# Performance work log

Measured on AMD Instinct MI355X. Metric: run time of the kernel, lower is better.

The kernel has to match this reference:

```python
import jax, jax.numpy as jnp
import numpy as np

F_FEAT = 310   # len(feature_names)
B = 2048       # samples; x has F_FEAT*B elements
H = 32         # sfp_neurons


def _uniform(key, shape, bound):
    return jax.random.uniform(key, shape, jnp.float32, -bound, bound)


def setup_inputs() -> dict:
    key = jax.random.key(0)
    ks = jax.random.split(key, 7)
    x = jax.random.normal(ks[0], (F_FEAT, B), dtype=jnp.float32)
    # Stacked per-feature MLP params (torch Linear default init: U(-1/sqrt(fan_in), +)).
    s1 = 1.0 / np.sqrt(F_FEAT - 1)
    s2 = 1.0 / np.sqrt(H)
    W1 = _uniform(ks[1], (F_FEAT, F_FEAT - 1, H), s1)  # (in, out) layout
    b1 = _uniform(ks[2], (F_FEAT, H), s1)
    W2 = _uniform(ks[3], (F_FEAT, H, H), s2)
    b2 = _uniform(ks[4], (F_FEAT, H), s2)
    W3 = _uniform(ks[5], (F_FEAT, H, H), s2)
    b3 = _uniform(ks[6], (F_FEAT, H), s2)
    return {"x": x, "W1": W1, "b1": b1, "W2": W2, "b2": b2, "W3": W3, "b3": b3}


def reference(x, W1, b1, W2, b2, W3, b3):
    F_, B_ = x.shape
    # Leave-one-out gather: for SFP i, rows [0..i-1, i+1..F-1] of x (feature-major),
    # then the original's view(-1, 1, F-1) reinterprets the flat buffer as (B, F-1).
    idx = jnp.arange(F_ - 1)[None, :]
    idx = idx + (idx >= jnp.arange(F_)[:, None])          # (F, F-1)
    X = x[idx].reshape(F_, B_, F_ - 1)                    # (F, B, F-1) grouped inputs
    h = jax.nn.relu(jnp.einsum('fbk,fkh->fbh', X, W1) + b1[:, None, :])
    h = jax.nn.relu(jnp.einsum('fbh,fhg->fbg', h, W2) + b2[:, None, :])
    h = jax.nn.relu(jnp.einsum('fbh,fhg->fbg', h, W3) + b3[:, None, :])  # (F, B, H)
    # torch.cat of per-SFP .view(-1) == row-major flatten of (F, B, H)
    return h.reshape(-1)
```

## Files before the change

kernel.cpp:

```cpp
#include <hip/hip_runtime.h>

namespace {

constexpr int F_FEAT = 310;
constexpr int KDIM   = 309;
constexpr int BSZ    = 2048;
constexpr int HDIM   = 32;
constexpr int NCH    = 10;
constexpr int NX     = F_FEAT * BSZ;

constexpr int    NBLK8    = NX / 8 + 2;
constexpr size_t CSTR_B   = (size_t)NBLK8 * 16;
constexpr size_t XC_BYTES = CSTR_B * 8;
constexpr size_t W1T_FSTR = 32 * 320 * 2;
constexpr size_t W1T_OFF  = XC_BYTES;
constexpr size_t W2T_OFF  = W1T_OFF + (size_t)F_FEAT * W1T_FSTR;
constexpr size_t WT_FSTR  = 32 * 32 * 2;
constexpr size_t W3T_OFF  = W2T_OFF + (size_t)F_FEAT * WT_FSTR;
constexpr size_t WS_NEED  = W3T_OFF + (size_t)F_FEAT * WT_FSTR;

constexpr int NBX      = (NBLK8 + 255) / 256;
constexpr int CVT_XBLK = NBX * 8;
constexpr int CVT_BLK  = CVT_XBLK + F_FEAT * 6;

typedef __bf16 bf16x8 __attribute__((ext_vector_type(8)));
typedef float  f32x4  __attribute__((ext_vector_type(4)));

#define MFMA(a, b, c) __builtin_amdgcn_mfma_f32_16x16x32_bf16((a), (b), (c), 0, 0, 0)

__global__ __launch_bounds__(256) void cvt_all(
    const float* __restrict__ x,  const float* __restrict__ W1,
    const float* __restrict__ W2, const float* __restrict__ W3,
    char* __restrict__ ws)
{
    __shared__ float tile[64][33];
    const int b = blockIdx.x, tid = threadIdx.x;

    if (b < CVT_XBLK) {
        const int c = b / NBX, mb = b - c * NBX;
        const int m = mb * 256 + tid;
        if (m >= NBLK8) return;
        const int e0 = m * 8 - c;
        bf16x8 v;
        #pragma unroll
        for (int q = 0; q < 8; ++q) {
            const int i = e0 + q;
            v[q] = (__bf16)((i >= 0 && i < NX) ? x[i] : 0.f);
        }
        *(bf16x8*)(ws + (size_t)c * CSTR_B + (size_t)m * 16) = v;
        return;
    }

    const int wb = b - CVT_XBLK;
    const int fi = wb / 6, part = wb - fi * 6;

    if (part < 5) {
        const float* Wg = W1 + (size_t)fi * KDIM * HDIM;
        const int row = tid >> 2;
        const int c8  = (tid & 3) * 8;
        const int k   = part * 64 + row;
        float4 f0 = make_float4(0,0,0,0), f1 = f0;
        if (k < KDIM) {
            f0 = *(const float4*)&Wg[k * HDIM + c8];
            f1 = *(const float4*)&Wg[k * HDIM + c8 + 4];
        }
        tile[row][c8+0] = f0.x; tile[row][c8+1] = f0.y;
        tile[row][c8+2] = f0.z; tile[row][c8+3] = f0.w;
        tile[row][c8+4] = f1.x; tile[row][c8+5] = f1.y;
        tile[row][c8+6] = f1.z; tile[row][c8+7] = f1.w;
        __syncthreads();
        const int h = tid & 31, kq = (tid >> 5) * 8;
        bf16x8 o;
        #pragma unroll
        for (int j = 0; j < 8; ++j) o[j] = (__bf16)tile[kq + j][h];
        const int boff = (h * 640 + part * 128 + kq * 2) ^ ((h & 7) << 4);
        *(bf16x8*)(ws + W1T_OFF + (size_t)fi * W1T_FSTR + (size_t)boff) = o;
    } else {
        const int kl = tid >> 3, h4 = (tid & 7) * 4;
        const int h = tid & 31, kq = (tid >> 5) * 8;
        {
            const float* Wg = W2 + (size_t)fi * HDIM * HDIM;
            float4 f = *(const float4*)&Wg[kl * HDIM + h4];
            tile[kl][h4+0] = f.x; tile[kl][h4+1] = f.y;
            tile[kl][h4+2] = f.z; tile[kl][h4+3] = f.w;
            __syncthreads();
            if (tid < 128) {
                bf16x8 o;
                #pragma unroll
                for (int j = 0; j < 8; ++j) o[j] = (__bf16)tile[kq + j][h];
                *(bf16x8*)(ws + W2T_OFF + (size_t)fi * WT_FSTR + (size_t)(h * 32 + kq) * 2) = o;
            }
            __syncthreads();
        }
        {
            const float* Wg = W3 + (size_t)fi * HDIM * HDIM;
            float4 f = *(const float4*)&Wg[kl * HDIM + h4];
            tile[kl][h4+0] = f.x; tile[kl][h4+1] = f.y;
            tile[kl][h4+2] = f.z; tile[kl][h4+3] = f.w;
            __syncthreads();
            if (tid < 128) {
                bf16x8 o;
                #pragma unroll
                for (int j = 0; j < 8; ++j) o[j] = (__bf16)tile[kq + j][h];
                *(bf16x8*)(ws + W3T_OFF + (size_t)fi * WT_FSTR + (size_t)(h * 32 + kq) * 2) = o;
            }
        }
    }
}

template<bool FAST>
__global__ __launch_bounds__(256, 4) void sfp3(
    const float* __restrict__ x,
    const float* __restrict__ W1, const float* __restrict__ b1,
    const float* __restrict__ W2, const float* __restrict__ b2,
    const float* __restrict__ W3, const float* __restrict__ b3,
    const char* __restrict__ ws, float* __restrict__ out)
{
    __shared__ __attribute__((aligned(16))) __bf16 W1s[32 * 320];
    __shared__ __attribute__((aligned(16))) __bf16 h1s[128 * 40];

    int fi, sb;
    if (FAST) {
        const int xc = blockIdx.x & 7, li = blockIdx.x >> 3;
        const int cnt = (xc < 6) ? 39 : 38;
        const int lf = li >> 4;
        if (lf >= cnt) return;
        fi = ((xc < 6) ? xc * 39 : 234 + (xc - 6) * 38) + lf;
        sb = li & 15;
    } else {
        fi = blockIdx.x >> 4; sb = blockIdx.x & 15;
    }

    const int tid = threadIdx.x, lane = tid & 63, wv = tid >> 6;
    const int l15 = lane & 15, l16 = lane >> 4;
    const int lk8 = l16 * 8, r0 = l16 * 4;
    const int b0 = sb << 7, iB = fi << 11;

    if (FAST) {
        const char* src = ws + W1T_OFF + (size_t)fi * W1T_FSTR;
        #pragma unroll
        for (int i = 0; i < 5; ++i) {
            const int off = i * 4096 + tid * 16;
            *(bf16x8*)((char*)W1s + off) = *(const bf16x8*)(src + off);
        }
        __syncthreads();
    }

    const float b1v0 = b1[fi*HDIM + l15], b1v1 = b1[fi*HDIM + 16 + l15];
    const float b2v0 = b2[fi*HDIM + l15], b2v1 = b2[fi*HDIM + 16 + l15];
    const float b3v0 = b3[fi*HDIM + l15], b3v1 = b3[fi*HDIM + 16 + l15];

    bf16x8 w2a, w2b, w3a, w3b;
    if (FAST) {
        const char* p2 = ws + W2T_OFF + (size_t)fi * WT_FSTR;
        const char* p3 = ws + W3T_OFF + (size_t)fi * WT_FSTR;
        w2a = *(const bf16x8*)(p2 + (size_t)(l15 * 32 + lk8) * 2);
        w2b = *(const bf16x8*)(p2 + (size_t)((16 + l15) * 32 + lk8) * 2);
        w3a = *(const bf16x8*)(p3 + (size_t)(l15 * 32 + lk8) * 2);
        w3b = *(const bf16x8*)(p3 + (size_t)((16 + l15) * 32 + lk8) * 2);
    } else {
        #pragma unroll
        for (int q = 0; q < 8; ++q) {
            const size_t base = (size_t)fi * HDIM * HDIM + (lk8 + q) * HDIM;
            w2a[q] = (__bf16)W2[base + l15];      w2b[q] = (__bf16)W2[base + 16 + l15];
            w3a[q] = (__bf16)W3[base + l15];      w3b[q] = (__bf16)W3[base + 16 + l15];
        }
    }

    const int mrow = wv * 32;
    const int lin0 = (b0 + mrow + l15) * KDIM + lk8;
    const int lin1 = lin0 + 16 * KDIM;
    const char* base0 = ws;
    const char* base1 = ws;
    if (FAST) {
        const int c80 = (-lin0) & 7, c81 = (-lin1) & 7;
        base0 = ws + (size_t)c80 * CSTR_B + (size_t)(lin0 + c80) * 2;
        base1 = ws + (size_t)c81 * CSTR_B + (size_t)(lin1 + c81) * 2;
    }

    auto fragA = [&](const char* base, int lin) -> bf16x8 {
        if (FAST) {
            if (__builtin_expect((unsigned)(iB - 1 - lin) < 7u, 0)) {
                bf16x8 r;
                #pragma unroll
                for (int q = 0; q < 8; ++q) {
                    int i = lin + q; i += (i >= iB) ? BSZ : 0;
                    r[q] = *(const __bf16*)(ws + (size_t)i * 2);
                }
                return r;
            }
            return *(const bf16x8*)(base + ((lin >= iB) ? 4096 : 0));
        } else {
            bf16x8 r;
            #pragma unroll
            for (int q = 0; q < 8; ++q) {
                int i = lin + q; i += (i >= iB) ? BSZ : 0;
                i = (i < NX) ? i : (NX - 1);
                r[q] = (__bf16)x[i];
            }
            return r;
        }
    };

    auto fragW1 = [&](int c, int hrow) -> bf16x8 {
        if (FAST) {
            const int boff = (hrow * 640 + c * 64 + l16 * 16) ^ ((hrow & 7) << 4);
            return *(const bf16x8*)((const char*)W1s + boff);
        } else {
            const float* Wg = W1 + (size_t)fi * KDIM * HDIM;
            bf16x8 r;
            #pragma unroll
            for (int q = 0; q < 8; ++q) {
                const int k = c * 32 + lk8 + q;
                r[q] = (__bf16)((k < KDIM) ? Wg[k * HDIM + hrow] : 0.f);
            }
            return r;
        }
    };

    f32x4 acc00 = {0,0,0,0}, acc01 = {0,0,0,0}, acc10 = {0,0,0,0}, acc11 = {0,0,0,0};

    bf16x8 aC0 = fragA(base0,      lin0);
    bf16x8 aC1 = fragA(base1,      lin1);
    bf16x8 aN0 = fragA(base0 + 64, lin0 + 32);
    bf16x8 aN1 = fragA(base1 + 64, lin1 + 32);
    #pragma unroll
    for (int c = 0; c < NCH; ++c) {
        bf16x8 aF0, aF1;
        if (c + 2 < NCH) {
            aF0 = fragA(base0 + 64 * (c + 2), lin0 + 32 * (c + 2));
            aF1 = fragA(base1 + 64 * (c + 2), lin1 + 32 * (c + 2));
        }
        bf16x8 w0 = fragW1(c, l15), w1 = fragW1(c, 16 + l15);
        acc00 = MFMA(aC0, w0, acc00);
        acc01 = MFMA(aC0, w1, acc01);
        acc10 = MFMA(aC1, w0, acc10);
        acc11 = MFMA(aC1, w1, acc11);
        aC0 = aN0; aC1 = aN1; aN0 = aF0; aN1 = aF1;
    }

    constexpr int LDA = 40;
    #pragma unroll
    for (int r = 0; r < 4; ++r) {
        float v;
        v = acc00[r] + b1v0; h1s[(mrow +      r0 + r)*LDA +      l15] = (__bf16)(v > 0.f ? v : 0.f);
        v = acc01[r] + b1v1; h1s[(mrow +      r0 + r)*LDA + 16 + l15] = (__bf16)(v > 0.f ? v : 0.f);
        v = acc10[r] + b1v0; h1s[(mrow + 16 + r0 + r)*LDA +      l15] = (__bf16)(v > 0.f ? v : 0.f);
        v = acc11[r] + b1v1; h1s[(mrow + 16 + r0 + r)*LDA + 16 + l15] = (__bf16)(v > 0.f ? v : 0.f);
    }

    const f32x4 z = {0,0,0,0};
    f32x4 c200, c201, c210, c211;
    {
        bf16x8 ha0 = *(const bf16x8*)&h1s[(mrow +      l15)*LDA + lk8];
        bf16x8 ha1 = *(const bf16x8*)&h1s[(mrow + 16 + l15)*LDA + lk8];
        c200 = MFMA(ha0, w2a, z); c201 = MFMA(ha0, w2b, z);
        c210 = MFMA(ha1, w2a, z); c211 = MFMA(ha1, w2b, z);
    }
    #pragma unroll
    for (int r = 0; r < 4; ++r) {
        float v;
        v = c200[r] + b2v0; h1s[(mrow +      r0 + r)*LDA +      l15] = (__bf16)(v > 0.f ? v : 0.f);
        v = c201[r] + b2v1; h1s[(mrow +      r0 + r)*LDA + 16 + l15] = (__bf16)(v > 0.f ? v : 0.f);
        v = c210[r] + b2v0; h1s[(mrow + 16 + r0 + r)*LDA +      l15] = (__bf16)(v > 0.f ? v : 0.f);
        v = c211[r] + b2v1; h1s[(mrow + 16 + r0 + r)*LDA + 16 + l15] = (__bf16)(v > 0.f ? v : 0.f);
    }

    f32x4 c300, c301, c310, c311;
    {
        bf16x8 ha0 = *(const bf16x8*)&h1s[(mrow +      l15)*LDA + lk8];
        bf16x8 ha1 = *(const bf16x8*)&h1s[(mrow + 16 + l15)*LDA + lk8];
        c300 = MFMA(ha0, w3a, z); c301 = MFMA(ha0, w3b, z);
        c310 = MFMA(ha1, w3a, z); c311 = MFMA(ha1, w3b, z);
    }

    const size_t orow = (size_t)(fi * BSZ + b0 + mrow);
    #pragma unroll
    for (int r = 0; r < 4; ++r) {
        float v;
        v = c300[r] + b3v0; out[(orow +      r0 + r)*HDIM +      l15] = v > 0.f ? v : 0.f;
        v = c301[r] + b3v1; out[(orow +      r0 + r)*HDIM + 16 + l15] = v > 0.f ? v : 0.f;
        v = c310[r] + b3v0; out[(orow + 16 + r0 + r)*HDIM +      l15] = v > 0.f ? v : 0.f;
        v = c311[r] + b3v1; out[(orow + 16 + r0 + r)*HDIM + 16 + l15] = v > 0.f ? v : 0.f;
    }
}

}

extern "C" void kernel_launch(void* const* d_in, const int* in_sizes, int n_in,
                              void* d_out, int out_size, void* d_ws, size_t ws_size,
                              hipStream_t stream) {
    const float* x  = (const float*)d_in[0];
    const float* W1 = (const float*)d_in[1];
    const float* b1 = (const float*)d_in[2];
    const float* W2 = (const float*)d_in[3];
    const float* b2 = (const float*)d_in[4];
    const float* W3 = (const float*)d_in[5];
    const float* b3 = (const float*)d_in[6];
    float* out = (float*)d_out;
    char* ws = (char*)d_ws;

    const bool fast = (ws != nullptr) && (ws_size >= WS_NEED);
    if (fast) {
        hipLaunchKernelGGL(cvt_all, dim3(CVT_BLK), dim3(256), 0, stream, x, W1, W2, W3, ws);
        hipLaunchKernelGGL((sfp3<true>), dim3(8 * 39 * 16), dim3(256), 0, stream,
                           x, W1, b1, W2, b2, W3, b3, ws, out);
    } else {
        hipLaunchKernelGGL((sfp3<false>), dim3(F_FEAT * 16), dim3(256), 0, stream,
                           x, W1, b1, W2, b2, W3, b3, ws, out);
    }
}
```

Measured before the change: 70.93 us.

## Double rows per block to amortize W1 staging and weight loads

Each block now covers 256 samples instead of 128, so each wave computes four 16-row M tiles instead of two. The per-feature W1 copy into shared memory and the W2/W3 fragment loads are amortized over twice the work, and the grid is halved. The A-fragment prefetch depth drops from two chunks to one. In exchange, register pressure rises from 8 accumulators plus more A fragments, shared memory for h1 doubles, and the smaller grid gives fewer blocks to hide latency.

```diff
diff --git a/kernel.cpp b/kernel.cpp
--- a/kernel.cpp
+++ b/kernel.cpp
@@ -109,7 +109,7 @@
 }
 
 template<bool FAST>
-__global__ __launch_bounds__(256, 4) void sfp3(
+__global__ __launch_bounds__(256, 4) void sfp4(
     const float* __restrict__ x,
     const float* __restrict__ W1, const float* __restrict__ b1,
     const float* __restrict__ W2, const float* __restrict__ b2,
@@ -117,24 +117,25 @@
     const char* __restrict__ ws, float* __restrict__ out)
 {
     __shared__ __attribute__((aligned(16))) __bf16 W1s[32 * 320];
-    __shared__ __attribute__((aligned(16))) __bf16 h1s[128 * 40];
+    __shared__ __attribute__((aligned(16))) __bf16 h1s[256 * 40];
 
     int fi, sb;
     if (FAST) {
         const int xc = blockIdx.x & 7, li = blockIdx.x >> 3;
         const int cnt = (xc < 6) ? 39 : 38;
-        const int lf = li >> 4;
+        const int lf = li >> 3;
         if (lf >= cnt) return;
         fi = ((xc < 6) ? xc * 39 : 234 + (xc - 6) * 38) + lf;
-        sb = li & 15;
+        sb = li & 7;
     } else {
-        fi = blockIdx.x >> 4; sb = blockIdx.x & 15;
+        fi = blockIdx.x >> 3; sb = blockIdx.x & 7;
     }
 
     const int tid = threadIdx.x, lane = tid & 63, wv = tid >> 6;
     const int l15 = lane & 15, l16 = lane >> 4;
     const int lk8 = l16 * 8, r0 = l16 * 4;
-    const int b0 = sb << 7, iB = fi << 11;
+    const int b0 = sb << 8, iB = fi << 11;
+    const int mrow = wv * 64;
 
     if (FAST) {
         const char* src = ws + W1T_OFF + (size_t)fi * W1T_FSTR;
@@ -167,34 +168,36 @@
         }
     }
 
-    const int mrow = wv * 32;
-    const int lin0 = (b0 + mrow + l15) * KDIM + lk8;
-    const int lin1 = lin0 + 16 * KDIM;
-    const char* base0 = ws;
-    const char* base1 = ws;
-    if (FAST) {
-        const int c80 = (-lin0) & 7, c81 = (-lin1) & 7;
-        base0 = ws + (size_t)c80 * CSTR_B + (size_t)(lin0 + c80) * 2;
-        base1 = ws + (size_t)c81 * CSTR_B + (size_t)(lin1 + c81) * 2;
-    }
-
-    auto fragA = [&](const char* base, int lin) -> bf16x8 {
+    int lin[4];
+    const char* base[4];
+    #pragma unroll
+    for (int m = 0; m < 4; ++m) {
+        lin[m] = (b0 + mrow + 16 * m + l15) * KDIM + lk8;
         if (FAST) {
-            if (__builtin_expect((unsigned)(iB - 1 - lin) < 7u, 0)) {
+            const int c8 = (-lin[m]) & 7;
+            base[m] = ws + (size_t)c8 * CSTR_B + (size_t)(lin[m] + c8) * 2;
+        } else {
+            base[m] = ws;
+        }
+    }
+
+    auto fragA = [&](const char* bp, int li_) -> bf16x8 {
+        if (FAST) {
+            if (__builtin_expect((unsigned)(iB - 1 - li_) < 7u, 0)) {
                 bf16x8 r;
                 #pragma unroll
                 for (int q = 0; q < 8; ++q) {
-                    int i = lin + q; i += (i >= iB) ? BSZ : 0;
+                    int i = li_ + q; i += (i >= iB) ? BSZ : 0;
                     r[q] = *(const __bf16*)(ws + (size_t)i * 2);
                 }
                 return r;
             }
-            return *(const bf16x8*)(base + ((lin >= iB) ? 4096 : 0));
+            return *(const bf16x8*)(bp + ((li_ >= iB) ? 4096 : 0));
         } else {
             bf16x8 r;
             #pragma unroll
             for (int q = 0; q < 8; ++q) {
-                int i = lin + q; i += (i >= iB) ? BSZ : 0;
+                int i = li_ + q; i += (i >= iB) ? BSZ : 0;
                 i = (i < NX) ? i : (NX - 1);
                 r[q] = (__bf16)x[i];
             }
@@ -218,70 +221,70 @@
         }
     };
 
-    f32x4 acc00 = {0,0,0,0}, acc01 = {0,0,0,0}, acc10 = {0,0,0,0}, acc11 = {0,0,0,0};
-
-    bf16x8 aC0 = fragA(base0,      lin0);
-    bf16x8 aC1 = fragA(base1,      lin1);
-    bf16x8 aN0 = fragA(base0 + 64, lin0 + 32);
-    bf16x8 aN1 = fragA(base1 + 64, lin1 + 32);
+    f32x4 acc[4][2];
+    #pragma unroll
+    for (int m = 0; m < 4; ++m) { acc[m][0] = {0,0,0,0}; acc[m][1] = {0,0,0,0}; }
+
+    bf16x8 aC[4], aN[4];
+    #pragma unroll
+    for (int m = 0; m < 4; ++m) aC[m] = fragA(base[m], lin[m]);
+
     #pragma unroll
     for (int c = 0; c < NCH; ++c) {
-        bf16x8 aF0, aF1;
-        if (c + 2 < NCH) {
-            aF0 = fragA(base0 + 64 * (c + 2), lin0 + 32 * (c + 2));
-            aF1 = fragA(base1 + 64 * (c + 2), lin1 + 32 * (c + 2));
-        }
-        bf16x8 w0 = fragW1(c, l15), w1 = fragW1(c, 16 + l15);
-        acc00 = MFMA(aC0, w0, acc00);
-        acc01 = MFMA(aC0, w1, acc01);
-        acc10 = MFMA(aC1, w0, acc10);
-        acc11 = MFMA(aC1, w1, acc11);
-        aC0 = aN0; aC1 = aN1; aN0 = aF0; aN1 = aF1;
+        if (c + 1 < NCH) {
+            #pragma unroll
+            for (int m = 0; m < 4; ++m)
+                aN[m] = fragA(base[m] + 64 * (c + 1), lin[m] + 32 * (c + 1));
+        }
+        const bf16x8 w0 = fragW1(c, l15), w1 = fragW1(c, 16 + l15);
+        #pragma unroll
+        for (int m = 0; m < 4; ++m) {
+            acc[m][0] = MFMA(aC[m], w0, acc[m][0]);
+            acc[m][1] = MFMA(aC[m], w1, acc[m][1]);
+        }
+        #pragma unroll
+        for (int m = 0; m < 4; ++m) aC[m] = aN[m];
     }
 
     constexpr int LDA = 40;
     #pragma unroll
-    for (int r = 0; r < 4; ++r) {
-        float v;
-        v = acc00[r] + b1v0; h1s[(mrow +      r0 + r)*LDA +      l15] = (__bf16)(v > 0.f ? v : 0.f);
-        v = acc01[r] + b1v1; h1s[(mrow +      r0 + r)*LDA + 16 + l15] = (__bf16)(v > 0.f ? v : 0.f);
-        v = acc10[r] + b1v0; h1s[(mrow + 16 + r0 + r)*LDA +      l15] = (__bf16)(v > 0.f ? v : 0.f);
-        v = acc11[r] + b1v1; h1s[(mrow + 16 + r0 + r)*LDA + 16 + l15] = (__bf16)(v > 0.f ? v : 0.f);
-    }
+    for (int m = 0; m < 4; ++m)
+        #pragma unroll
+        for (int r = 0; r < 4; ++r) {
+            float v;
+            v = acc[m][0][r] + b1v0; h1s[(mrow + 16*m + r0 + r)*LDA +      l15] = (__bf16)(v > 0.f ? v : 0.f);
+            v = acc[m][1][r] + b1v1; h1s[(mrow + 16*m + r0 + r)*LDA + 16 + l15] = (__bf16)(v > 0.f ? v : 0.f);
+        }
 
     const f32x4 z = {0,0,0,0};
-    f32x4 c200, c201, c210, c211;
-    {
-        bf16x8 ha0 = *(const bf16x8*)&h1s[(mrow +      l15)*LDA + lk8];
-        bf16x8 ha1 = *(const bf16x8*)&h1s[(mrow + 16 + l15)*LDA + lk8];
-        c200 = MFMA(ha0, w2a, z); c201 = MFMA(ha0, w2b, z);
-        c210 = MFMA(ha1, w2a, z); c211 = MFMA(ha1, w2b, z);
-    }
-    #pragma unroll
-    for (int r = 0; r < 4; ++r) {
-        float v;
-        v = c200[r] + b2v0; h1s[(mrow +      r0 + r)*LDA +      l15] = (__bf16)(v > 0.f ? v : 0.f);
-        v = c201[r] + b2v1; h1s[(mrow +      r0 + r)*LDA + 16 + l15] = (__bf16)(v > 0.f ? v : 0.f);
-        v = c210[r] + b2v0; h1s[(mrow + 16 + r0 + r)*LDA +      l15] = (__bf16)(v > 0.f ? v : 0.f);
-        v = c211[r] + b2v1; h1s[(mrow + 16 + r0 + r)*LDA + 16 + l15] = (__bf16)(v > 0.f ? v : 0.f);
-    }
-
-    f32x4 c300, c301, c310, c311;
-    {
-        bf16x8 ha0 = *(const bf16x8*)&h1s[(mrow +      l15)*LDA + lk8];
-        bf16x8 ha1 = *(const bf16x8*)&h1s[(mrow + 16 + l15)*LDA + lk8];
-        c300 = MFMA(ha0, w3a, z); c301 = MFMA(ha0, w3b, z);
-        c310 = MFMA(ha1, w3a, z); c311 = MFMA(ha1, w3b, z);
-    }
+    f32x4 c2[4][2];
+    #pragma unroll
+    for (int m = 0; m < 4; ++m) {
+        bf16x8 ha = *(const bf16x8*)&h1s[(mrow + 16*m + l15)*LDA + lk8];
+        c2[m][0] = MFMA(ha, w2a, z);
+        c2[m][1] = MFMA(ha, w2b, z);
+    }
+    #pragma unroll
+    for (int m = 0; m < 4; ++m)
+        #pragma unroll
+        for (int r = 0; r < 4; ++r) {
+            float v;
+            v = c2[m][0][r] + b2v0; h1s[(mrow + 16*m + r0 + r)*LDA +      l15] = (__bf16)(v > 0.f ? v : 0.f);
+            v = c2[m][1][r] + b2v1; h1s[(mrow + 16*m + r0 + r)*LDA + 16 + l15] = (__bf16)(v > 0.f ? v : 0.f);
+        }
 
     const size_t orow = (size_t)(fi * BSZ + b0 + mrow);
     #pragma unroll
-    for (int r = 0; r < 4; ++r) {
-        float v;
-        v = c300[r] + b3v0; out[(orow +      r0 + r)*HDIM +      l15] = v > 0.f ? v : 0.f;
-        v = c301[r] + b3v1; out[(orow +      r0 + r)*HDIM + 16 + l15] = v > 0.f ? v : 0.f;
-        v = c310[r] + b3v0; out[(orow + 16 + r0 + r)*HDIM +      l15] = v > 0.f ? v : 0.f;
-        v = c311[r] + b3v1; out[(orow + 16 + r0 + r)*HDIM + 16 + l15] = v > 0.f ? v : 0.f;
+    for (int m = 0; m < 4; ++m) {
+        bf16x8 ha = *(const bf16x8*)&h1s[(mrow + 16*m + l15)*LDA + lk8];
+        f32x4 c30 = MFMA(ha, w3a, z);
+        f32x4 c31 = MFMA(ha, w3b, z);
+        #pragma unroll
+        for (int r = 0; r < 4; ++r) {
+            float v;
+            v = c30[r] + b3v0; out[(orow + 16*m + r0 + r)*HDIM +      l15] = v > 0.f ? v : 0.f;
+            v = c31[r] + b3v1; out[(orow + 16*m + r0 + r)*HDIM + 16 + l15] = v > 0.f ? v : 0.f;
+        }
     }
 }
 
@@ -303,10 +306,10 @@
     const bool fast = (ws != nullptr) && (ws_size >= WS_NEED);
     if (fast) {
         hipLaunchKernelGGL(cvt_all, dim3(CVT_BLK), dim3(256), 0, stream, x, W1, W2, W3, ws);
-        hipLaunchKernelGGL((sfp3<true>), dim3(8 * 39 * 16), dim3(256), 0, stream,
+        hipLaunchKernelGGL((sfp4<true>), dim3(8 * 39 * 8), dim3(256), 0, stream,
                            x, W1, b1, W2, b2, W3, b3, ws, out);
     } else {
-        hipLaunchKernelGGL((sfp3<false>), dim3(F_FEAT * 16), dim3(256), 0, stream,
+        hipLaunchKernelGGL((sfp4<false>), dim3(F_FEAT * 8), dim3(256), 0, stream,
                            x, W1, b1, W2, b2, W3, b3, ws, out);
     }
 }
```

Measured after the change: 72.75 us. 2.6% more time.

## Alias h1 buffer onto W1 shared tile, raise occupancy, prefetch A and W1 frags

Applied to the files above, without the earlier changes.

Merges the W1 and h1 shared-memory buffers into one aliased buffer, with a barrier added before h1 overwrites the W1 tile. This cuts LDS per block so launch_bounds can ask for 7 blocks per CU instead of 4. The first A-fragment global loads are issued before the W1 copy into shared memory to overlap latency, and W1 fragments are software-prefetched one chunk ahead. The cost is an extra __syncthreads and more register pressure under the tighter launch bound.

```diff
diff --git a/kernel.cpp b/kernel.cpp
--- a/kernel.cpp
+++ b/kernel.cpp
@@ -109,15 +109,14 @@
 }
 
 template<bool FAST>
-__global__ __launch_bounds__(256, 4) void sfp3(
+__global__ __launch_bounds__(256, 7) void sfp8(
     const float* __restrict__ x,
     const float* __restrict__ W1, const float* __restrict__ b1,
     const float* __restrict__ W2, const float* __restrict__ b2,
     const float* __restrict__ W3, const float* __restrict__ b3,
     const char* __restrict__ ws, float* __restrict__ out)
 {
-    __shared__ __attribute__((aligned(16))) __bf16 W1s[32 * 320];
-    __shared__ __attribute__((aligned(16))) __bf16 h1s[128 * 40];
+    __shared__ __attribute__((aligned(16))) __bf16 shbuf[32 * 320];
 
     int fi, sb;
     if (FAST) {
@@ -136,12 +135,68 @@
     const int lk8 = l16 * 8, r0 = l16 * 4;
     const int b0 = sb << 7, iB = fi << 11;
 
+    const int mrow = wv * 32;
+    const int lin0 = (b0 + mrow + l15) * KDIM + lk8;
+    const int lin1 = lin0 + 16 * KDIM;
+    const char* base0 = ws;
+    const char* base1 = ws;
+    if (FAST) {
+        const int c80 = (-lin0) & 7, c81 = (-lin1) & 7;
+        base0 = ws + (size_t)c80 * CSTR_B + (size_t)(lin0 + c80) * 2;
+        base1 = ws + (size_t)c81 * CSTR_B + (size_t)(lin1 + c81) * 2;
+    }
+
+    auto fragA = [&](const char* base, int lin) -> bf16x8 {
+        if (FAST) {
+            if (__builtin_expect((unsigned)(iB - 1 - lin) < 7u, 0)) {
+                bf16x8 r;
+                #pragma unroll
+                for (int q = 0; q < 8; ++q) {
+                    int i = lin + q; i += (i >= iB) ? BSZ : 0;
+                    r[q] = *(const __bf16*)(ws + (size_t)i * 2);
+                }
+                return r;
+            }
+            return *(const bf16x8*)(base + ((lin >= iB) ? 4096 : 0));
+        } else {
+            bf16x8 r;
+            #pragma unroll
+            for (int q = 0; q < 8; ++q) {
+                int i = lin + q; i += (i >= iB) ? BSZ : 0;
+                i = (i < NX) ? i : (NX - 1);
+                r[q] = (__bf16)x[i];
+            }
+            return r;
+        }
+    };
+
+    auto fragW1 = [&](int c, int hrow) -> bf16x8 {
+        if (FAST) {
+            const int boff = (hrow * 640 + c * 64 + l16 * 16) ^ ((hrow & 7) << 4);
+            return *(const bf16x8*)((const char*)shbuf + boff);
+        } else {
+            const float* Wg = W1 + (size_t)fi * KDIM * HDIM;
+            bf16x8 r;
+            #pragma unroll
+            for (int q = 0; q < 8; ++q) {
+                const int k = c * 32 + lk8 + q;
+                r[q] = (__bf16)((k < KDIM) ? Wg[k * HDIM + hrow] : 0.f);
+            }
+            return r;
+        }
+    };
+
+    bf16x8 a0 = fragA(base0, lin0);
+    bf16x8 a1 = fragA(base1, lin1);
+    bf16x8 aN0 = fragA(base0 + 64, lin0 + 32);
+    bf16x8 aN1 = fragA(base1 + 64, lin1 + 32);
+
     if (FAST) {
         const char* src = ws + W1T_OFF + (size_t)fi * W1T_FSTR;
         #pragma unroll
         for (int i = 0; i < 5; ++i) {
             const int off = i * 4096 + tid * 16;
-            *(bf16x8*)((char*)W1s + off) = *(const bf16x8*)(src + off);
+            *(bf16x8*)((char*)shbuf + off) = *(const bf16x8*)(src + off);
         }
         __syncthreads();
     }
@@ -161,69 +216,15 @@
     } else {
         #pragma unroll
         for (int q = 0; q < 8; ++q) {
-            const size_t base = (size_t)fi * HDIM * HDIM + (lk8 + q) * HDIM;
-            w2a[q] = (__bf16)W2[base + l15];      w2b[q] = (__bf16)W2[base + 16 + l15];
-            w3a[q] = (__bf16)W3[base + l15];      w3b[q] = (__bf16)W3[base + 16 + l15];
-        }
-    }
-
-    const int mrow = wv * 32;
-    const int lin0 = (b0 + mrow + l15) * KDIM + lk8;
-    const int lin1 = lin0 + 16 * KDIM;
-    const char* base0 = ws;
-    const char* base1 = ws;
-    if (FAST) {
-        const int c80 = (-lin0) & 7, c81 = (-lin1) & 7;
-        base0 = ws + (size_t)c80 * CSTR_B + (size_t)(lin0 + c80) * 2;
-        base1 = ws + (size_t)c81 * CSTR_B + (size_t)(lin1 + c81) * 2;
-    }
-
-    auto fragA = [&](const char* base, int lin) -> bf16x8 {
-        if (FAST) {
-            if (__builtin_expect((unsigned)(iB - 1 - lin) < 7u, 0)) {
-                bf16x8 r;
-                #pragma unroll
-                for (int q = 0; q < 8; ++q) {
-                    int i = lin + q; i += (i >= iB) ? BSZ : 0;
-                    r[q] = *(const __bf16*)(ws + (size_t)i * 2);
-                }
-                return r;
-            }
-            return *(const bf16x8*)(base + ((lin >= iB) ? 4096 : 0));
-        } else {
-            bf16x8 r;
-            #pragma unroll
-            for (int q = 0; q < 8; ++q) {
-                int i = lin + q; i += (i >= iB) ? BSZ : 0;
-                i = (i < NX) ? i : (NX - 1);
-                r[q] = (__bf16)x[i];
-            }
-            return r;
-        }
-    };
-
-    auto fragW1 = [&](int c, int hrow) -> bf16x8 {
-        if (FAST) {
-            const int boff = (hrow * 640 + c * 64 + l16 * 16) ^ ((hrow & 7) << 4);
-            return *(const bf16x8*)((const char*)W1s + boff);
-        } else {
-            const float* Wg = W1 + (size_t)fi * KDIM * HDIM;
-            bf16x8 r;
-            #pragma unroll
-            for (int q = 0; q < 8; ++q) {
-                const int k = c * 32 + lk8 + q;
-                r[q] = (__bf16)((k < KDIM) ? Wg[k * HDIM + hrow] : 0.f);
-            }
-            return r;
-        }
-    };
+            const size_t base2 = (size_t)fi * HDIM * HDIM + (lk8 + q) * HDIM;
+            w2a[q] = (__bf16)W2[base2 + l15];      w2b[q] = (__bf16)W2[base2 + 16 + l15];
+            w3a[q] = (__bf16)W3[base2 + l15];      w3b[q] = (__bf16)W3[base2 + 16 + l15];
+        }
+    }
 
     f32x4 acc00 = {0,0,0,0}, acc01 = {0,0,0,0}, acc10 = {0,0,0,0}, acc11 = {0,0,0,0};
 
-    bf16x8 aC0 = fragA(base0,      lin0);
-    bf16x8 aC1 = fragA(base1,      lin1);
-    bf16x8 aN0 = fragA(base0 + 64, lin0 + 32);
-    bf16x8 aN1 = fragA(base1 + 64, lin1 + 32);
+    bf16x8 w0 = fragW1(0, l15), w1 = fragW1(0, 16 + l15);
     #pragma unroll
     for (int c = 0; c < NCH; ++c) {
         bf16x8 aF0, aF1;
@@ -231,15 +232,20 @@
             aF0 = fragA(base0 + 64 * (c + 2), lin0 + 32 * (c + 2));
             aF1 = fragA(base1 + 64 * (c + 2), lin1 + 32 * (c + 2));
         }
-        bf16x8 w0 = fragW1(c, l15), w1 = fragW1(c, 16 + l15);
-        acc00 = MFMA(aC0, w0, acc00);
-        acc01 = MFMA(aC0, w1, acc01);
-        acc10 = MFMA(aC1, w0, acc10);
-        acc11 = MFMA(aC1, w1, acc11);
-        aC0 = aN0; aC1 = aN1; aN0 = aF0; aN1 = aF1;
-    }
-
+        bf16x8 nw0, nw1;
+        if (c + 1 < NCH) { nw0 = fragW1(c + 1, l15); nw1 = fragW1(c + 1, 16 + l15); }
+        acc00 = MFMA(a0, w0, acc00);
+        acc01 = MFMA(a0, w1, acc01);
+        acc10 = MFMA(a1, w0, acc10);
+        acc11 = MFMA(a1, w1, acc11);
+        a0 = aN0; a1 = aN1; aN0 = aF0; aN1 = aF1;
+        w0 = nw0; w1 = nw1;
+    }
+
+    __syncthreads();
+    __bf16* h1s = shbuf;
     constexpr int LDA = 40;
+
     #pragma unroll
     for (int r = 0; r < 4; ++r) {
         float v;
@@ -303,10 +309,10 @@
     const bool fast = (ws != nullptr) && (ws_size >= WS_NEED);
     if (fast) {
         hipLaunchKernelGGL(cvt_all, dim3(CVT_BLK), dim3(256), 0, stream, x, W1, W2, W3, ws);
-        hipLaunchKernelGGL((sfp3<true>), dim3(8 * 39 * 16), dim3(256), 0, stream,
+        hipLaunchKernelGGL((sfp8<true>), dim3(8 * 39 * 16), dim3(256), 0, stream,
                            x, W1, b1, W2, b2, W3, b3, ws, out);
     } else {
-        hipLaunchKernelGGL((sfp3<false>), dim3(F_FEAT * 16), dim3(256), 0, stream,
+        hipLaunchKernelGGL((sfp8<false>), dim3(F_FEAT * 16), dim3(256), 0, stream,
                            x, W1, b1, W2, b2, W3, b3, ws, out);
     }
 }
```

After: 99.40 us. 1.4x slower.
